# Kernel tuning notes

Measured on AMD Instinct MI355X. Metric: run time of the kernel, lower is better.

The kernel has to match this reference:

```python
import jax, jax.numpy as jnp
import numpy as np

GAMMA = 1.0
BIG = 1e10  # finite stand-in for +inf boundary; exp(-BIG) underflows to exactly 0 (grad-safe)


def setup_inputs() -> dict:
    key = jax.random.key(0)
    k1, k2 = jax.random.split(key)
    B, L, C = 64, 1024, 64
    x = jax.random.normal(k1, (B, L, C), dtype=jnp.float32)
    y = jax.random.normal(k2, (B, L, C), dtype=jnp.float32)
    return {"x": x, "y": y}


def _soft_dtw(x, y, gamma=GAMMA):
    B, L, C = x.shape
    # squared-euclidean pairwise cost, scaled by 1/gamma (matches torch code)
    x2 = jnp.sum(x * x, axis=-1)[:, :, None]            # [B,L,1]
    y2 = jnp.sum(y * y, axis=-1)[:, None, :]            # [B,1,L]
    D = (x2 + y2 - 2.0 * jnp.einsum('blc,bmc->blm', x, y)) / gamma  # [B,L,L]

    # Anti-diagonal wavefront DP over the (L+2)x(L+2) R matrix.
    # r_d[i] holds R[i, d-i] for the diagonal i+j=d, i in 0..L+1.
    n = L + 2
    ii = jnp.arange(n)
    i_idx = jnp.clip(ii - 1, 0, L - 1)
    r_prev2 = jnp.full((B, n), BIG, dtype=x.dtype).at[:, 0].set(0.0)  # diag d=0: R[0,0]=0
    r_prev1 = jnp.full((B, n), BIG, dtype=x.dtype)                    # diag d=1: all boundary
    big_col = jnp.full((B, 1), BIG, dtype=x.dtype)

    def step(carry, d):
        rp2, rp1 = carry
        jj = d - ii
        valid = (ii >= 1) & (ii <= L) & (jj >= 1) & (jj <= L)
        j_idx = jnp.clip(jj - 1, 0, L - 1)
        d_vals = D[:, i_idx, j_idx]                                   # [B,n] cost along diagonal
        r_diag = jnp.concatenate([big_col, rp2[:, :-1]], axis=1)      # R[i-1, j-1]
        r_up   = jnp.concatenate([big_col, rp1[:, :-1]], axis=1)      # R[i-1, j]
        r_left = rp1                                                  # R[i,   j-1]
        z = jnp.stack([-r_diag, -r_up, -r_left], axis=-1)             # [B,n,3]
        zmax = jnp.max(z, axis=-1)
        softmin = -(jnp.log(jnp.sum(jnp.exp(z - zmax[..., None]), axis=-1)) + zmax)
        new = jnp.where(valid[None, :], d_vals + softmin, BIG)
        return (rp1, new), None

    (_, r_last), _ = jax.lax.scan(step, (r_prev2, r_prev1), jnp.arange(2, 2 * L + 1))
    # last diagonal is d=2L; R[L,L] sits at index i=L
    return r_last[:, L] * gamma


def reference(x, y):
    return _soft_dtw(x, y)
```

## Files before the change

kernel.cpp:

```cpp
#include <hip/hip_runtime.h>


typedef unsigned short ushort_t;
typedef __attribute__((ext_vector_type(8))) short short8;
typedef __attribute__((ext_vector_type(4))) float f32x4;
typedef __attribute__((ext_vector_type(4))) unsigned short ushort4v;

constexpr int B_ = 64, L_ = 1024, C_ = 64;
constexpr int DSTR = 130;
constexpr int HBSTR = 1280;

#define BIGV 1e10f
#define INV_LN2 1.44269504088896340736f
#define LN2F 0.69314718055994530942f
#define DPP_WAVE_SHL1 0x130
#define DPP_WAVE_SHR1 0x138

static __device__ __forceinline__ ushort_t f2bf(float f) {
  unsigned u = __builtin_bit_cast(unsigned, f);
  unsigned r = (u + 0x7fffu + ((u >> 16) & 1u)) >> 16;
  return (ushort_t)r;
}
static __device__ __forceinline__ float exp2_(float x) {
  float r; asm("v_exp_f32 %0, %1" : "=v"(r) : "v"(x)); return r;
}
static __device__ __forceinline__ float log2_(float x) {
  float r; asm("v_log_f32 %0, %1" : "=v"(r) : "v"(x)); return r;
}
static __device__ __forceinline__ unsigned cvt_pk_bf16(float lo, float hi) {
  unsigned r; asm("v_cvt_pk_bf16_f32 %0, %1, %2" : "=v"(r) : "v"(lo), "v"(hi)); return r;
}
static __device__ __forceinline__ float dpp_shr1(float old, float src) {
  return __builtin_bit_cast(float, __builtin_amdgcn_update_dpp(
      __builtin_bit_cast(int, old), __builtin_bit_cast(int, src),
      DPP_WAVE_SHR1, 0xF, 0xF, false));
}
static __device__ __forceinline__ float dpp_shl1(float v) {
  return __builtin_bit_cast(float, __builtin_amdgcn_update_dpp(
      __builtin_bit_cast(int, v), __builtin_bit_cast(int, v),
      DPP_WAVE_SHL1, 0xF, 0xF, false));
}

__global__ __launch_bounds__(256) void prep_kernel(
    const float* __restrict__ x, const float* __restrict__ y,
    ushort_t* __restrict__ xb, ushort_t* __restrict__ yb,
    float* __restrict__ x2, float* __restrict__ y2, int* __restrict__ flagsG)
{
  if (blockIdx.x == 0 && threadIdx.x < 192) flagsG[threadIdx.x] = 0;
  const int lane = threadIdx.x & 63;
  const int sub = lane >> 4;
  const int cg  = lane & 15;
  const int wv = (blockIdx.x * blockDim.x + threadIdx.x) >> 6;
  const int nw = (gridDim.x * blockDim.x) >> 6;
  const int totalGroups = (2 * B_ * L_) >> 2;
  for (int g = wv; g < totalGroups; g += nw) {
    int r = g * 4 + sub;
    const float* src; ushort_t* dst; float* nrm;
    if (r < B_ * L_) { src = x; dst = xb; nrm = x2; }
    else             { r -= B_ * L_; src = y; dst = yb; nrm = y2; }
    const float4 v = *(const float4*)(src + (size_t)r * C_ + cg * 4);
    ushort4v p;
    p.x = f2bf(v.x); p.y = f2bf(v.y); p.z = f2bf(v.z); p.w = f2bf(v.w);
    *(ushort4v*)(dst + (size_t)r * C_ + cg * 4) = p;
    float s = v.x*v.x + v.y*v.y + v.z*v.z + v.w*v.w;
    s += __shfl_xor(s, 1); s += __shfl_xor(s, 2);
    s += __shfl_xor(s, 4); s += __shfl_xor(s, 8);
    if (cg == 0) nrm[r] = s * INV_LN2;
  }
}

template<int HDST, bool FIRST>
static __device__ __forceinline__ void dp_chunk(
    const int t, const int lane, float& cur, float& dgp, float hvv,
    const float zsel, const ushort_t* __restrict__ DtwLane,
    float* __restrict__ HbDst, float* __restrict__ HXB)
{
  const unsigned* pw = (const unsigned*)(DtwLane + ((t << 6) & 127));
  const int cb = (t << 6) - 63;
  unsigned a0 = pw[0], a1 = pw[1], b0 = pw[2], b1 = pw[3];

  auto step = [&](unsigned dw, int k, int u) -> float {
    float dv = __builtin_bit_cast(float, (k & 1) ? (dw & 0xffff0000u) : (dw << 16));
    float up = dpp_shr1(hvv, cur);
    float dg = dgp, lf = cur;
    if constexpr (FIRST) {
      bool at0 = (u == lane);
      dg = at0 ? zsel : dg;
      lf = at0 ? BIGV : lf;
    }
    float mn = fminf(fminf(up, dg), lf);
    float e = exp2_(mn - up) + exp2_(mn - dg) + exp2_(mn - lf);
    float nv = (dv + mn) - log2_(e);
    dgp = up;
    hvv = dpp_shl1(hvv);
    if constexpr (FIRST) { if (u >= lane) cur = nv; }
    else cur = nv;
    return nv;
  };
  auto flush4 = [&](int c0, float v0, float v1, float v2, float v3) {
    if constexpr (HDST == 0) {
      if (lane == 63) { HbDst[c0] = v0; HbDst[c0+1] = v1; HbDst[c0+2] = v2; HbDst[c0+3] = v3; }
    } else if constexpr (HDST == 1) {
      if (lane == 63) { HXB[c0] = v0; HXB[c0+1] = v1; HXB[c0+2] = v2; HXB[c0+3] = v3; }
    }
  };

  #pragma unroll 1
  for (int g = 0; g < 8; ++g) {
    const int u0 = g * 8;
    unsigned n0 = 0, n1 = 0, n2 = 0, n3 = 0;
    if (g < 7) {
      n0 = pw[u0/2 + 4]; n1 = pw[u0/2 + 5]; n2 = pw[u0/2 + 6]; n3 = pw[u0/2 + 7];
    }
    float v0 = step(a0, 0, u0 + 0);
    float v1 = step(a0, 1, u0 + 1);
    float v2 = step(a1, 0, u0 + 2);
    float v3 = step(a1, 1, u0 + 3);
    if constexpr (!FIRST) flush4(cb + u0, v0, v1, v2, v3);
    float v4 = step(b0, 0, u0 + 4);
    float v5 = step(b0, 1, u0 + 5);
    float v6 = step(b1, 0, u0 + 6);
    float v7 = step(b1, 1, u0 + 7);
    if constexpr (!FIRST) flush4(cb + u0 + 4, v4, v5, v6, v7);
    a0 = n0; a1 = n1; b0 = n2; b1 = n3;
    (void)v0; (void)v1; (void)v2; (void)v3; (void)v4; (void)v5; (void)v6; (void)v7;
  }
  if constexpr (FIRST) {
    if constexpr (HDST == 0) { if (lane == 63) HbDst[0] = cur; }
    else if constexpr (HDST == 1) { if (lane == 63) HXB[0] = cur; }
  }
}

template<int HDST>
static __device__ __forceinline__ void dp_tail(
    const int lane, float& cur, float& dgp,
    const ushort_t* __restrict__ DtwLane,
    float* __restrict__ HbDst, float* __restrict__ HXB)
{
  const unsigned* pw = (const unsigned*)(DtwLane);
  #pragma unroll 1
  for (int g = 0; g < 8; ++g) {
    unsigned w0 = pw[g*4], w1 = pw[g*4+1], w2 = pw[g*4+2], w3 = pw[g*4+3];
    #pragma unroll
    for (int k = 0; k < 8; ++k) {
      const int u = g * 8 + k;
      unsigned dw = (k < 2) ? w0 : (k < 4) ? w1 : (k < 6) ? w2 : w3;
      float dv = __builtin_bit_cast(float, (k & 1) ? (dw & 0xffff0000u) : (dw << 16));
      float up = dpp_shr1(BIGV, cur);
      float dg = dgp, lf = cur;
      float mn = fminf(fminf(up, dg), lf);
      float e = exp2_(mn - up) + exp2_(mn - dg) + exp2_(mn - lf);
      float nv = (dv + mn) - log2_(e);
      dgp = up;
      if (u < lane) {
        cur = nv;
        if constexpr (HDST == 0) { if (lane == 63) HbDst[961 + u] = nv; }
        else if constexpr (HDST == 1) { if (lane == 63) HXB[961 + u] = nv; }
      }
    }
  }
}

static __device__ __forceinline__ void spin_lds(int* f, int v) {
  int k = 0;
  while (__hip_atomic_load(f, __ATOMIC_ACQUIRE, __HIP_MEMORY_SCOPE_WORKGROUP) < v) {
    __builtin_amdgcn_s_sleep(1);
    if (++k > (1 << 26)) break;
  }
}
static __device__ __forceinline__ void spin_glb(int* f, int v) {
  int k = 0;
  while (__hip_atomic_load(f, __ATOMIC_ACQUIRE, __HIP_MEMORY_SCOPE_AGENT) < v) {
    __builtin_amdgcn_s_sleep(8);
    if (++k > (1 << 26)) break;
  }
}

template<int HSRC, int HDST>
static __device__ __forceinline__ void run_band(
    const ushort_t* __restrict__ xbB, const ushort_t* __restrict__ ybB,
    const float* __restrict__ x2B, const float* __restrict__ y2B,
    const float* __restrict__ HXin, float* __restrict__ HXout,
    int* __restrict__ fGin, int* __restrict__ fGout,
    ushort_t* __restrict__ Dtw, const float* __restrict__ HbSrc,
    float* __restrict__ HbDst, int* __restrict__ cin, int* __restrict__ cout,
    const int lane, const int W, float* __restrict__ outp)
{
  const int m = lane & 15, q = lane >> 4;
  const int i0 = W * 64;

  short8 af[4][2];
  #pragma unroll
  for (int mt = 0; mt < 4; ++mt)
    #pragma unroll
    for (int ks = 0; ks < 2; ++ks)
      af[mt][ks] = *(const short8*)(xbB + (size_t)(i0 + mt * 16 + m) * C_ + ks * 32 + q * 8);
  f32x4 x2q[4];
  #pragma unroll
  for (int mt = 0; mt < 4; ++mt) x2q[mt] = *(const f32x4*)(x2B + i0 + mt * 16 + q * 4);

  short8 bfr0[4], bfr1[4];
  auto load_bfr = [&](int tc) {
    const ushort_t* yb0 = ybB + (size_t)tc * 64 * C_;
    #pragma unroll
    for (int nt = 0; nt < 4; ++nt) {
      bfr0[nt] = *(const short8*)(yb0 + (size_t)(nt * 16 + m) * C_ + q * 8);
      bfr1[nt] = *(const short8*)(yb0 + (size_t)(nt * 16 + m) * C_ + 32 + q * 8);
    }
  };
  auto gram = [&](int tc) {
    const int cb = tc * 64;
    const float* y2j = y2B + cb;
    #pragma unroll
    for (int mt = 0; mt < 4; ++mt) {
      const int r0 = mt * 16 + q * 4;
      #pragma unroll
      for (int nt = 0; nt < 4; ++nt) {
        f32x4 acc = {0.f, 0.f, 0.f, 0.f};
        acc = __builtin_amdgcn_mfma_f32_16x16x32_bf16(af[mt][0], bfr0[nt], acc, 0, 0, 0);
        acc = __builtin_amdgcn_mfma_f32_16x16x32_bf16(af[mt][1], bfr1[nt], acc, 0, 0, 0);
        float y2v = y2j[nt * 16 + m];
        float d0 = fmaf(acc[0], -2.f * INV_LN2, x2q[mt][0] + y2v);
        float d1 = fmaf(acc[1], -2.f * INV_LN2, x2q[mt][1] + y2v);
        float d2 = fmaf(acc[2], -2.f * INV_LN2, x2q[mt][2] + y2v);
        float d3 = fmaf(acc[3], -2.f * INV_LN2, x2q[mt][3] + y2v);
        unsigned p01 = cvt_pk_bf16(d0, d1);
        unsigned p23 = cvt_pk_bf16(d2, d3);
        const int cs = cb + nt * 16 + m + r0;
        ushort_t* base = Dtw + r0 * DSTR;
        base[             ( cs      & 127)] = (ushort_t)p01;
        base[    DSTR  +  ((cs + 1) & 127)] = (ushort_t)(p01 >> 16);
        base[2 * DSTR  +  ((cs + 2) & 127)] = (ushort_t)p23;
        base[3 * DSTR  +  ((cs + 3) & 127)] = (ushort_t)(p23 >> 16);
      }
    }
  };

  float cur = 0.f, dgp = BIGV;
  const float zsel = (W == 0 && lane == 0) ? 0.f : BIGV;
  const ushort_t* DtwLane = Dtw + lane * DSTR;

  load_bfr(0);
  gram(0);

  #pragma unroll 1
  for (int t = 0; t < 16; ++t) {
    if (t < 15) load_bfr(t + 1);
    float hvv;
    if constexpr (HSRC == 0) {
      hvv = BIGV;
    } else if constexpr (HSRC == 1) {
      spin_lds(cin, t + 1);
      hvv = HbSrc[(t << 6) + lane];
    } else {
      spin_glb(fGin, t + 1);
      hvv = HXin[(t << 6) + lane];
    }
    if (t == 0) dp_chunk<HDST, true >(0, lane, cur, dgp, hvv, zsel, DtwLane, HbDst, HXout);
    else        dp_chunk<HDST, false>(t, lane, cur, dgp, hvv, zsel, DtwLane, HbDst, HXout);
    if constexpr (HDST == 0) {
      if (lane == 0) __hip_atomic_store(cout, t, __ATOMIC_RELEASE, __HIP_MEMORY_SCOPE_WORKGROUP);
    } else if constexpr (HDST == 1) {
      if (lane == 0) __hip_atomic_store(fGout, t, __ATOMIC_RELEASE, __HIP_MEMORY_SCOPE_AGENT);
    }
    if (t < 15) gram(t + 1);
  }
  dp_tail<HDST>(lane, cur, dgp, DtwLane, HbDst, HXout);
  if constexpr (HDST == 0) {
    if (lane == 0) __hip_atomic_store(cout, 16, __ATOMIC_RELEASE, __HIP_MEMORY_SCOPE_WORKGROUP);
  } else if constexpr (HDST == 1) {
    if (lane == 0) __hip_atomic_store(fGout, 16, __ATOMIC_RELEASE, __HIP_MEMORY_SCOPE_AGENT);
  }
  if (W == 15 && lane == 63) *outp = cur * LN2F;
}

__global__ __launch_bounds__(256) void sdtw_kernel(
    const ushort_t* __restrict__ xb, const ushort_t* __restrict__ yb,
    const float* __restrict__ x2g, const float* __restrict__ y2g,
    float* __restrict__ HXg, int* __restrict__ flagsG,
    float* __restrict__ out)
{
  __shared__ ushort_t Dt[4][64 * DSTR];
  __shared__ float Hb[3][HBSTR];
  __shared__ int cflag[4];

  const int b = blockIdx.x & 63;
  const int sub = blockIdx.x >> 6;
  const int w = threadIdx.x >> 6;
  const int lane = threadIdx.x & 63;
  const int W = sub * 4 + w;

  if (threadIdx.x < 4) cflag[threadIdx.x] = 0;
  __syncthreads();

  const ushort_t* xbB = xb + (size_t)b * L_ * C_;
  const ushort_t* ybB = yb + (size_t)b * L_ * C_;
  const float* x2B = x2g + b * L_;
  const float* y2B = y2g + b * L_;
  const float* HXin = HXg + ((size_t)b * 3 + (sub - 1)) * L_;
  float* HXout      = HXg + ((size_t)b * 3 + sub) * L_;
  int* fGin  = flagsG + b * 3 + (sub - 1);
  int* fGout = flagsG + b * 3 + sub;
  ushort_t* Dtw = &Dt[w][0];
  const float* HbSrc = (w > 0) ? &Hb[w - 1][0] : &Hb[0][0];
  float* HbDst = (w < 3) ? &Hb[w][0] : &Hb[0][0];
  int* cin  = (w > 0) ? &cflag[w - 1] : &cflag[0];
  int* cout = (w < 3) ? &cflag[w] : &cflag[3];
  float* outp = out + b;

  if (sub == 0) {
    if (w == 0)      run_band<0, 0>(xbB, ybB, x2B, y2B, HXin, HXout, fGin, fGout, Dtw, HbSrc, HbDst, cin, cout, lane, W, outp);
    else if (w < 3)  run_band<1, 0>(xbB, ybB, x2B, y2B, HXin, HXout, fGin, fGout, Dtw, HbSrc, HbDst, cin, cout, lane, W, outp);
    else             run_band<1, 1>(xbB, ybB, x2B, y2B, HXin, HXout, fGin, fGout, Dtw, HbSrc, HbDst, cin, cout, lane, W, outp);
  } else if (sub < 3) {
    if (w == 0)      run_band<2, 0>(xbB, ybB, x2B, y2B, HXin, HXout, fGin, fGout, Dtw, HbSrc, HbDst, cin, cout, lane, W, outp);
    else if (w < 3)  run_band<1, 0>(xbB, ybB, x2B, y2B, HXin, HXout, fGin, fGout, Dtw, HbSrc, HbDst, cin, cout, lane, W, outp);
    else             run_band<1, 1>(xbB, ybB, x2B, y2B, HXin, HXout, fGin, fGout, Dtw, HbSrc, HbDst, cin, cout, lane, W, outp);
  } else {
    if (w == 0)      run_band<2, 0>(xbB, ybB, x2B, y2B, HXin, HXout, fGin, fGout, Dtw, HbSrc, HbDst, cin, cout, lane, W, outp);
    else if (w < 3)  run_band<1, 0>(xbB, ybB, x2B, y2B, HXin, HXout, fGin, fGout, Dtw, HbSrc, HbDst, cin, cout, lane, W, outp);
    else             run_band<1, 2>(xbB, ybB, x2B, y2B, HXin, HXout, fGin, fGout, Dtw, HbSrc, HbDst, cin, cout, lane, W, outp);
  }
}

extern "C" void kernel_launch(void* const* d_in, const int* in_sizes, int n_in,
                              void* d_out, int out_size, void* d_ws, size_t ws_size,
                              hipStream_t stream) {
  const float* x = (const float*)d_in[0];
  const float* y = (const float*)d_in[1];
  float* out = (float*)d_out;

  char* ws = (char*)d_ws;
  const size_t XB = (size_t)B_ * L_ * C_ * 2;
  const size_t NB = (size_t)B_ * L_ * 4;
  ushort_t* xb = (ushort_t*)ws;
  ushort_t* yb = (ushort_t*)(ws + XB);
  float* x2 = (float*)(ws + 2 * XB);
  float* y2 = (float*)(ws + 2 * XB + NB);
  float* HX = (float*)(ws + 2 * XB + 2 * NB);
  int* flagsG = (int*)(ws + 2 * XB + 2 * NB + (size_t)B_ * 3 * L_ * 4);

  prep_kernel<<<512, 256, 0, stream>>>(x, y, xb, yb, x2, y2, flagsG);
  sdtw_kernel<<<256, 256, 0, stream>>>(xb, yb, x2, y2, HX, flagsG, out);
}
```

Measured before the change: 355.3 us.

## Interleave Gram MFMA into DP steps and use fine-grained intra-block handoff flags

```diff
diff --git a/kernel.cpp b/kernel.cpp
--- a/kernel.cpp
+++ b/kernel.cpp
@@ -13,32 +13,28 @@
 #define BIGV 1e10f
 #define INV_LN2 1.44269504088896340736f
 #define LN2F 0.69314718055994530942f
-#define DPP_WAVE_SHL1 0x130
-#define DPP_WAVE_SHR1 0x138
+
+template<int N> struct IC { static constexpr int v = N; };
+template<int I, int N, class F>
+static __device__ __forceinline__ void sfor(F&& f) {
+  if constexpr (I < N) { f(IC<I>{}); sfor<I + 1, N>(f); }
+}
 
 static __device__ __forceinline__ ushort_t f2bf(float f) {
   unsigned u = __builtin_bit_cast(unsigned, f);
   unsigned r = (u + 0x7fffu + ((u >> 16) & 1u)) >> 16;
   return (ushort_t)r;
 }
-static __device__ __forceinline__ float exp2_(float x) {
-  float r; asm("v_exp_f32 %0, %1" : "=v"(r) : "v"(x)); return r;
-}
-static __device__ __forceinline__ float log2_(float x) {
-  float r; asm("v_log_f32 %0, %1" : "=v"(r) : "v"(x)); return r;
-}
 static __device__ __forceinline__ unsigned cvt_pk_bf16(float lo, float hi) {
   unsigned r; asm("v_cvt_pk_bf16_f32 %0, %1, %2" : "=v"(r) : "v"(lo), "v"(hi)); return r;
 }
 static __device__ __forceinline__ float dpp_shr1(float old, float src) {
   return __builtin_bit_cast(float, __builtin_amdgcn_update_dpp(
-      __builtin_bit_cast(int, old), __builtin_bit_cast(int, src),
-      DPP_WAVE_SHR1, 0xF, 0xF, false));
+      __builtin_bit_cast(int, old), __builtin_bit_cast(int, src), 0x138, 0xF, 0xF, false));
 }
 static __device__ __forceinline__ float dpp_shl1(float v) {
   return __builtin_bit_cast(float, __builtin_amdgcn_update_dpp(
-      __builtin_bit_cast(int, v), __builtin_bit_cast(int, v),
-      DPP_WAVE_SHL1, 0xF, 0xF, false));
+      __builtin_bit_cast(int, v), __builtin_bit_cast(int, v), 0x130, 0xF, 0xF, false));
 }
 
 __global__ __launch_bounds__(256) void prep_kernel(
@@ -69,98 +65,6 @@
   }
 }
 
-template<int HDST, bool FIRST>
-static __device__ __forceinline__ void dp_chunk(
-    const int t, const int lane, float& cur, float& dgp, float hvv,
-    const float zsel, const ushort_t* __restrict__ DtwLane,
-    float* __restrict__ HbDst, float* __restrict__ HXB)
-{
-  const unsigned* pw = (const unsigned*)(DtwLane + ((t << 6) & 127));
-  const int cb = (t << 6) - 63;
-  unsigned a0 = pw[0], a1 = pw[1], b0 = pw[2], b1 = pw[3];
-
-  auto step = [&](unsigned dw, int k, int u) -> float {
-    float dv = __builtin_bit_cast(float, (k & 1) ? (dw & 0xffff0000u) : (dw << 16));
-    float up = dpp_shr1(hvv, cur);
-    float dg = dgp, lf = cur;
-    if constexpr (FIRST) {
-      bool at0 = (u == lane);
-      dg = at0 ? zsel : dg;
-      lf = at0 ? BIGV : lf;
-    }
-    float mn = fminf(fminf(up, dg), lf);
-    float e = exp2_(mn - up) + exp2_(mn - dg) + exp2_(mn - lf);
-    float nv = (dv + mn) - log2_(e);
-    dgp = up;
-    hvv = dpp_shl1(hvv);
-    if constexpr (FIRST) { if (u >= lane) cur = nv; }
-    else cur = nv;
-    return nv;
-  };
-  auto flush4 = [&](int c0, float v0, float v1, float v2, float v3) {
-    if constexpr (HDST == 0) {
-      if (lane == 63) { HbDst[c0] = v0; HbDst[c0+1] = v1; HbDst[c0+2] = v2; HbDst[c0+3] = v3; }
-    } else if constexpr (HDST == 1) {
-      if (lane == 63) { HXB[c0] = v0; HXB[c0+1] = v1; HXB[c0+2] = v2; HXB[c0+3] = v3; }
-    }
-  };
-
-  #pragma unroll 1
-  for (int g = 0; g < 8; ++g) {
-    const int u0 = g * 8;
-    unsigned n0 = 0, n1 = 0, n2 = 0, n3 = 0;
-    if (g < 7) {
-      n0 = pw[u0/2 + 4]; n1 = pw[u0/2 + 5]; n2 = pw[u0/2 + 6]; n3 = pw[u0/2 + 7];
-    }
-    float v0 = step(a0, 0, u0 + 0);
-    float v1 = step(a0, 1, u0 + 1);
-    float v2 = step(a1, 0, u0 + 2);
-    float v3 = step(a1, 1, u0 + 3);
-    if constexpr (!FIRST) flush4(cb + u0, v0, v1, v2, v3);
-    float v4 = step(b0, 0, u0 + 4);
-    float v5 = step(b0, 1, u0 + 5);
-    float v6 = step(b1, 0, u0 + 6);
-    float v7 = step(b1, 1, u0 + 7);
-    if constexpr (!FIRST) flush4(cb + u0 + 4, v4, v5, v6, v7);
-    a0 = n0; a1 = n1; b0 = n2; b1 = n3;
-    (void)v0; (void)v1; (void)v2; (void)v3; (void)v4; (void)v5; (void)v6; (void)v7;
-  }
-  if constexpr (FIRST) {
-    if constexpr (HDST == 0) { if (lane == 63) HbDst[0] = cur; }
-    else if constexpr (HDST == 1) { if (lane == 63) HXB[0] = cur; }
-  }
-}
-
-template<int HDST>
-static __device__ __forceinline__ void dp_tail(
-    const int lane, float& cur, float& dgp,
-    const ushort_t* __restrict__ DtwLane,
-    float* __restrict__ HbDst, float* __restrict__ HXB)
-{
-  const unsigned* pw = (const unsigned*)(DtwLane);
-  #pragma unroll 1
-  for (int g = 0; g < 8; ++g) {
-    unsigned w0 = pw[g*4], w1 = pw[g*4+1], w2 = pw[g*4+2], w3 = pw[g*4+3];
-    #pragma unroll
-    for (int k = 0; k < 8; ++k) {
-      const int u = g * 8 + k;
-      unsigned dw = (k < 2) ? w0 : (k < 4) ? w1 : (k < 6) ? w2 : w3;
-      float dv = __builtin_bit_cast(float, (k & 1) ? (dw & 0xffff0000u) : (dw << 16));
-      float up = dpp_shr1(BIGV, cur);
-      float dg = dgp, lf = cur;
-      float mn = fminf(fminf(up, dg), lf);
-      float e = exp2_(mn - up) + exp2_(mn - dg) + exp2_(mn - lf);
-      float nv = (dv + mn) - log2_(e);
-      dgp = up;
-      if (u < lane) {
-        cur = nv;
-        if constexpr (HDST == 0) { if (lane == 63) HbDst[961 + u] = nv; }
-        else if constexpr (HDST == 1) { if (lane == 63) HXB[961 + u] = nv; }
-      }
-    }
-  }
-}
-
 static __device__ __forceinline__ void spin_lds(int* f, int v) {
   int k = 0;
   while (__hip_atomic_load(f, __ATOMIC_ACQUIRE, __HIP_MEMORY_SCOPE_WORKGROUP) < v) {
@@ -171,7 +75,7 @@
 static __device__ __forceinline__ void spin_glb(int* f, int v) {
   int k = 0;
   while (__hip_atomic_load(f, __ATOMIC_ACQUIRE, __HIP_MEMORY_SCOPE_AGENT) < v) {
-    __builtin_amdgcn_s_sleep(8);
+    __builtin_amdgcn_s_sleep(2);
     if (++k > (1 << 26)) break;
   }
 }
@@ -183,10 +87,11 @@
     const float* __restrict__ HXin, float* __restrict__ HXout,
     int* __restrict__ fGin, int* __restrict__ fGout,
     ushort_t* __restrict__ Dtw, const float* __restrict__ HbSrc,
-    float* __restrict__ HbDst, int* __restrict__ cin, int* __restrict__ cout,
+    float* __restrict__ HbDst, float* __restrict__ HScr,
+    int* __restrict__ cin, int* __restrict__ cout,
     const int lane, const int W, float* __restrict__ outp)
 {
-  const int m = lane & 15, q = lane >> 4;
+  const int m = lane & 15, q = lane >> 4, l7 = lane & 7;
   const int i0 = W * 64;
 
   short8 af[4][2];
@@ -200,77 +105,189 @@
   for (int mt = 0; mt < 4; ++mt) x2q[mt] = *(const f32x4*)(x2B + i0 + mt * 16 + q * 4);
 
   short8 bfr0[4], bfr1[4];
+  f32x4 y2r = {0.f, 0.f, 0.f, 0.f};
   auto load_bfr = [&](int tc) {
     const ushort_t* yb0 = ybB + (size_t)tc * 64 * C_;
     #pragma unroll
     for (int nt = 0; nt < 4; ++nt) {
       bfr0[nt] = *(const short8*)(yb0 + (size_t)(nt * 16 + m) * C_ + q * 8);
       bfr1[nt] = *(const short8*)(yb0 + (size_t)(nt * 16 + m) * C_ + 32 + q * 8);
-    }
-  };
-  auto gram = [&](int tc) {
-    const int cb = tc * 64;
-    const float* y2j = y2B + cb;
-    #pragma unroll
-    for (int mt = 0; mt < 4; ++mt) {
-      const int r0 = mt * 16 + q * 4;
+      y2r[nt] = y2B[tc * 64 + nt * 16 + m];
+    }
+  };
+
+  auto gram_pair = [&](auto PC, const int gcb) {
+    constexpr int p = decltype(PC)::v;
+    constexpr int mt = p >> 2;
+    constexpr int nt = p & 3;
+    f32x4 acc = {0.f, 0.f, 0.f, 0.f};
+    acc = __builtin_amdgcn_mfma_f32_16x16x32_bf16(af[mt][0], bfr0[nt], acc, 0, 0, 0);
+    acc = __builtin_amdgcn_mfma_f32_16x16x32_bf16(af[mt][1], bfr1[nt], acc, 0, 0, 0);
+    const float y2v = y2r[nt];
+    float d0 = fmaf(acc[0], -2.f * INV_LN2, x2q[mt][0] + y2v);
+    float d1 = fmaf(acc[1], -2.f * INV_LN2, x2q[mt][1] + y2v);
+    float d2 = fmaf(acc[2], -2.f * INV_LN2, x2q[mt][2] + y2v);
+    float d3 = fmaf(acc[3], -2.f * INV_LN2, x2q[mt][3] + y2v);
+    unsigned p01 = cvt_pk_bf16(d0, d1);
+    unsigned p23 = cvt_pk_bf16(d2, d3);
+    const int rr = mt * 16 + q * 4;
+    const int cs = gcb + nt * 16 + m + rr;
+    ushort_t* base = Dtw + rr * DSTR;
+    base[            ( cs      & 127)] = (ushort_t)p01;
+    base[    DSTR +  ((cs + 1) & 127)] = (ushort_t)(p01 >> 16);
+    base[2 * DSTR +  ((cs + 2) & 127)] = (ushort_t)p23;
+    base[3 * DSTR +  ((cs + 3) & 127)] = (ushort_t)(p23 >> 16);
+  };
+
+  float cur = 0.f, dgp = BIGV, hvv = BIGV;
+  const float zsel = (W == 0 && lane == 0) ? 0.0f : BIGV;
+  const ushort_t* DtLane = Dtw + lane * DSTR;
+
+  auto dp_chunk = [&](auto FC, auto GC, const int t) {
+    constexpr bool FIRST  = decltype(FC)::v != 0;
+    constexpr bool DOGRAM = decltype(GC)::v != 0;
+    const unsigned* pw = (const unsigned*)(DtLane + ((t << 6) & 127));
+    const int cb = (t << 6) - 63;
+    const int gcb = (t + 1) << 6;
+
+    if constexpr (HSRC == 2) {
+      spin_glb(fGin, t + 1);
+      HScr[lane] = HXin[(t << 6) + lane];
+    }
+
+    unsigned d0 = pw[0], d1 = pw[1], d2 = pw[2], d3 = pw[3];
+
+    auto step = [&](unsigned dw, int k, int u) -> float {
+      float dv = __builtin_bit_cast(float, (k & 1) ? (dw & 0xffff0000u) : (dw << 16));
+      float up = dpp_shr1(hvv, cur);
+      float dg = dgp, lf = cur;
+      if constexpr (FIRST) {
+        bool at0 = (u == lane);
+        dg = at0 ? zsel : dg;
+        lf = at0 ? BIGV : lf;
+      }
+      float mn = fminf(fminf(up, dg), lf);
+      float e = __builtin_amdgcn_exp2f(mn - up) + __builtin_amdgcn_exp2f(mn - dg)
+              + __builtin_amdgcn_exp2f(mn - lf);
+      float nv = (dv + mn) - __builtin_amdgcn_logf(e);
+      dgp = up;
+      if constexpr (HSRC != 0) hvv = dpp_shl1(hvv);
+      if constexpr (FIRST) { if (u >= lane) cur = nv; }
+      else cur = nv;
+      return nv;
+    };
+    auto flush4 = [&](int c0, float v0, float v1, float v2, float v3) {
+      if constexpr (HDST == 0) {
+        if (lane == 63) { HbDst[c0] = v0; HbDst[c0+1] = v1; HbDst[c0+2] = v2; HbDst[c0+3] = v3; }
+      } else if constexpr (HDST == 1) {
+        if (lane == 63) { HXout[c0] = v0; HXout[c0+1] = v1; HXout[c0+2] = v2; HXout[c0+3] = v3; }
+      }
+    };
+
+    sfor<0, 8>([&](auto GG) {
+      constexpr int g = decltype(GG)::v;
+      if constexpr (HSRC == 1) {
+        if constexpr ((g & 1) == 0) spin_lds(cin, (t << 6) + (g << 3) + 16);
+        hvv = HbSrc[(t << 6) + (g << 3) + l7];
+      } else if constexpr (HSRC == 2) {
+        hvv = HScr[(g << 3) + l7];
+      }
+      unsigned n0 = 0, n1 = 0, n2 = 0, n3 = 0;
+      if constexpr (g < 7) {
+        n0 = pw[4*g+4]; n1 = pw[4*g+5]; n2 = pw[4*g+6]; n3 = pw[4*g+7];
+      }
+      const int u0 = g << 3;
+      float v0 = step(d0, 0, u0 + 0);
+      float v1 = step(d0, 1, u0 + 1);
+      float v2 = step(d1, 0, u0 + 2);
+      float v3 = step(d1, 1, u0 + 3);
+      if constexpr (!FIRST) flush4(cb + u0, v0, v1, v2, v3);
+      float v4 = step(d2, 0, u0 + 4);
+      float v5 = step(d2, 1, u0 + 5);
+      float v6 = step(d3, 0, u0 + 6);
+      float v7 = step(d3, 1, u0 + 7);
+      if constexpr (!FIRST) flush4(cb + u0 + 4, v4, v5, v6, v7);
+      if constexpr (DOGRAM) {
+        gram_pair(IC<2*g>{}, gcb);
+        gram_pair(IC<2*g+1>{}, gcb);
+      }
+      if constexpr (HDST == 0 && !FIRST) {
+        if constexpr ((g & 1) == 1) {
+          if (lane == 0)
+            __hip_atomic_store(cout, (t << 6) + (g << 3) - 55,
+                               __ATOMIC_RELEASE, __HIP_MEMORY_SCOPE_WORKGROUP);
+        }
+      }
+      d0 = n0; d1 = n1; d2 = n2; d3 = n3;
+      (void)v0;(void)v1;(void)v2;(void)v3;(void)v4;(void)v5;(void)v6;(void)v7;
+    });
+    if constexpr (FIRST) {
+      if (lane == 63) {
+        if constexpr (HDST == 0) HbDst[0] = cur;
+        else if constexpr (HDST == 1) HXout[0] = cur;
+      }
+      if constexpr (HDST == 0) {
+        if (lane == 0)
+          __hip_atomic_store(cout, 1, __ATOMIC_RELEASE, __HIP_MEMORY_SCOPE_WORKGROUP);
+      }
+    }
+  };
+
+  auto signal_glb = [&](int v) {
+    if constexpr (HDST == 1) {
+      if (lane == 0) __hip_atomic_store(fGout, v, __ATOMIC_RELEASE, __HIP_MEMORY_SCOPE_AGENT);
+    }
+  };
+
+  auto dp_tail = [&]() {
+    const unsigned* pw = (const unsigned*)DtLane;
+    #pragma unroll 1
+    for (int g = 0; g < 8; ++g) {
+      unsigned w0 = pw[g*4], w1 = pw[g*4+1], w2 = pw[g*4+2], w3 = pw[g*4+3];
       #pragma unroll
-      for (int nt = 0; nt < 4; ++nt) {
-        f32x4 acc = {0.f, 0.f, 0.f, 0.f};
-        acc = __builtin_amdgcn_mfma_f32_16x16x32_bf16(af[mt][0], bfr0[nt], acc, 0, 0, 0);
-        acc = __builtin_amdgcn_mfma_f32_16x16x32_bf16(af[mt][1], bfr1[nt], acc, 0, 0, 0);
-        float y2v = y2j[nt * 16 + m];
-        float d0 = fmaf(acc[0], -2.f * INV_LN2, x2q[mt][0] + y2v);
-        float d1 = fmaf(acc[1], -2.f * INV_LN2, x2q[mt][1] + y2v);
-        float d2 = fmaf(acc[2], -2.f * INV_LN2, x2q[mt][2] + y2v);
-        float d3 = fmaf(acc[3], -2.f * INV_LN2, x2q[mt][3] + y2v);
-        unsigned p01 = cvt_pk_bf16(d0, d1);
-        unsigned p23 = cvt_pk_bf16(d2, d3);
-        const int cs = cb + nt * 16 + m + r0;
-        ushort_t* base = Dtw + r0 * DSTR;
-        base[             ( cs      & 127)] = (ushort_t)p01;
-        base[    DSTR  +  ((cs + 1) & 127)] = (ushort_t)(p01 >> 16);
-        base[2 * DSTR  +  ((cs + 2) & 127)] = (ushort_t)p23;
-        base[3 * DSTR  +  ((cs + 3) & 127)] = (ushort_t)(p23 >> 16);
-      }
-    }
-  };
-
-  float cur = 0.f, dgp = BIGV;
-  const float zsel = (W == 0 && lane == 0) ? 0.f : BIGV;
-  const ushort_t* DtwLane = Dtw + lane * DSTR;
+      for (int k = 0; k < 8; ++k) {
+        const int u = g * 8 + k;
+        unsigned dw = (k < 2) ? w0 : (k < 4) ? w1 : (k < 6) ? w2 : w3;
+        float dv = __builtin_bit_cast(float, (k & 1) ? (dw & 0xffff0000u) : (dw << 16));
+        float up = dpp_shr1(BIGV, cur);
+        float dg = dgp, lf = cur;
+        float mn = fminf(fminf(up, dg), lf);
+        float e = __builtin_amdgcn_exp2f(mn - up) + __builtin_amdgcn_exp2f(mn - dg)
+                + __builtin_amdgcn_exp2f(mn - lf);
+        float nv = (dv + mn) - __builtin_amdgcn_logf(e);
+        dgp = up;
+        if (u < lane) {
+          cur = nv;
+          if (lane == 63) {
+            if constexpr (HDST == 0) HbDst[961 + u] = nv;
+            else if constexpr (HDST == 1) HXout[961 + u] = nv;
+          }
+        }
+      }
+      if constexpr (HDST == 0) {
+        if (lane == 0)
+          __hip_atomic_store(cout, (g < 7) ? (969 + 8 * g) : 1024,
+                             __ATOMIC_RELEASE, __HIP_MEMORY_SCOPE_WORKGROUP);
+      }
+    }
+  };
 
   load_bfr(0);
-  gram(0);
-
+  sfor<0, 16>([&](auto PC) { gram_pair(PC, 0); });
+
+  load_bfr(1);
+  dp_chunk(IC<1>{}, IC<1>{}, 0);
+  signal_glb(0);
   #pragma unroll 1
-  for (int t = 0; t < 16; ++t) {
-    if (t < 15) load_bfr(t + 1);
-    float hvv;
-    if constexpr (HSRC == 0) {
-      hvv = BIGV;
-    } else if constexpr (HSRC == 1) {
-      spin_lds(cin, t + 1);
-      hvv = HbSrc[(t << 6) + lane];
-    } else {
-      spin_glb(fGin, t + 1);
-      hvv = HXin[(t << 6) + lane];
-    }
-    if (t == 0) dp_chunk<HDST, true >(0, lane, cur, dgp, hvv, zsel, DtwLane, HbDst, HXout);
-    else        dp_chunk<HDST, false>(t, lane, cur, dgp, hvv, zsel, DtwLane, HbDst, HXout);
-    if constexpr (HDST == 0) {
-      if (lane == 0) __hip_atomic_store(cout, t, __ATOMIC_RELEASE, __HIP_MEMORY_SCOPE_WORKGROUP);
-    } else if constexpr (HDST == 1) {
-      if (lane == 0) __hip_atomic_store(fGout, t, __ATOMIC_RELEASE, __HIP_MEMORY_SCOPE_AGENT);
-    }
-    if (t < 15) gram(t + 1);
-  }
-  dp_tail<HDST>(lane, cur, dgp, DtwLane, HbDst, HXout);
-  if constexpr (HDST == 0) {
-    if (lane == 0) __hip_atomic_store(cout, 16, __ATOMIC_RELEASE, __HIP_MEMORY_SCOPE_WORKGROUP);
-  } else if constexpr (HDST == 1) {
-    if (lane == 0) __hip_atomic_store(fGout, 16, __ATOMIC_RELEASE, __HIP_MEMORY_SCOPE_AGENT);
-  }
+  for (int t = 1; t <= 14; ++t) {
+    load_bfr(t + 1);
+    dp_chunk(IC<0>{}, IC<1>{}, t);
+    signal_glb(t);
+  }
+  dp_chunk(IC<0>{}, IC<0>{}, 15);
+  signal_glb(15);
+  dp_tail();
+  signal_glb(16);
   if (W == 15 && lane == 63) *outp = cur * LN2F;
 }
 
@@ -282,6 +299,7 @@
 {
   __shared__ ushort_t Dt[4][64 * DSTR];
   __shared__ float Hb[3][HBSTR];
+  __shared__ float HScr[64];
   __shared__ int cflag[4];
 
   const int b = blockIdx.x & 63;
@@ -297,10 +315,10 @@
   const ushort_t* ybB = yb + (size_t)b * L_ * C_;
   const float* x2B = x2g + b * L_;
   const float* y2B = y2g + b * L_;
-  const float* HXin = HXg + ((size_t)b * 3 + (sub - 1)) * L_;
-  float* HXout      = HXg + ((size_t)b * 3 + sub) * L_;
-  int* fGin  = flagsG + b * 3 + (sub - 1);
-  int* fGout = flagsG + b * 3 + sub;
+  const float* HXin = HXg + ((size_t)b * 3 + (sub > 0 ? sub - 1 : 0)) * L_;
+  float* HXout      = HXg + ((size_t)b * 3 + (sub < 3 ? sub : 2)) * L_;
+  int* fGin  = flagsG + b * 3 + (sub > 0 ? sub - 1 : 0);
+  int* fGout = flagsG + b * 3 + (sub < 3 ? sub : 2);
   ushort_t* Dtw = &Dt[w][0];
   const float* HbSrc = (w > 0) ? &Hb[w - 1][0] : &Hb[0][0];
   float* HbDst = (w < 3) ? &Hb[w][0] : &Hb[0][0];
@@ -309,17 +327,17 @@
   float* outp = out + b;
 
   if (sub == 0) {
-    if (w == 0)      run_band<0, 0>(xbB, ybB, x2B, y2B, HXin, HXout, fGin, fGout, Dtw, HbSrc, HbDst, cin, cout, lane, W, outp);
-    else if (w < 3)  run_band<1, 0>(xbB, ybB, x2B, y2B, HXin, HXout, fGin, fGout, Dtw, HbSrc, HbDst, cin, cout, lane, W, outp);
-    else             run_band<1, 1>(xbB, ybB, x2B, y2B, HXin, HXout, fGin, fGout, Dtw, HbSrc, HbDst, cin, cout, lane, W, outp);
+    if (w == 0)      run_band<0, 0>(xbB, ybB, x2B, y2B, HXin, HXout, fGin, fGout, Dtw, HbSrc, HbDst, HScr, cin, cout, lane, W, outp);
+    else if (w < 3)  run_band<1, 0>(xbB, ybB, x2B, y2B, HXin, HXout, fGin, fGout, Dtw, HbSrc, HbDst, HScr, cin, cout, lane, W, outp);
+    else             run_band<1, 1>(xbB, ybB, x2B, y2B, HXin, HXout, fGin, fGout, Dtw, HbSrc, HbDst, HScr, cin, cout, lane, W, outp);
   } else if (sub < 3) {
-    if (w == 0)      run_band<2, 0>(xbB, ybB, x2B, y2B, HXin, HXout, fGin, fGout, Dtw, HbSrc, HbDst, cin, cout, lane, W, outp);
-    else if (w < 3)  run_band<1, 0>(xbB, ybB, x2B, y2B, HXin, HXout, fGin, fGout, Dtw, HbSrc, HbDst, cin, cout, lane, W, outp);
-    else             run_band<1, 1>(xbB, ybB, x2B, y2B, HXin, HXout, fGin, fGout, Dtw, HbSrc, HbDst, cin, cout, lane, W, outp);
+    if (w == 0)      run_band<2, 0>(xbB, ybB, x2B, y2B, HXin, HXout, fGin, fGout, Dtw, HbSrc, HbDst, HScr, cin, cout, lane, W, outp);
+    else if (w < 3)  run_band<1, 0>(xbB, ybB, x2B, y2B, HXin, HXout, fGin, fGout, Dtw, HbSrc, HbDst, HScr, cin, cout, lane, W, outp);
+    else             run_band<1, 1>(xbB, ybB, x2B, y2B, HXin, HXout, fGin, fGout, Dtw, HbSrc, HbDst, HScr, cin, cout, lane, W, outp);
   } else {
-    if (w == 0)      run_band<2, 0>(xbB, ybB, x2B, y2B, HXin, HXout, fGin, fGout, Dtw, HbSrc, HbDst, cin, cout, lane, W, outp);
-    else if (w < 3)  run_band<1, 0>(xbB, ybB, x2B, y2B, HXin, HXout, fGin, fGout, Dtw, HbSrc, HbDst, cin, cout, lane, W, outp);
-    else             run_band<1, 2>(xbB, ybB, x2B, y2B, HXin, HXout, fGin, fGout, Dtw, HbSrc, HbDst, cin, cout, lane, W, outp);
+    if (w == 0)      run_band<2, 0>(xbB, ybB, x2B, y2B, HXin, HXout, fGin, fGout, Dtw, HbSrc, HbDst, HScr, cin, cout, lane, W, outp);
+    else if (w < 3)  run_band<1, 0>(xbB, ybB, x2B, y2B, HXin, HXout, fGin, fGout, Dtw, HbSrc, HbDst, HScr, cin, cout, lane, W, outp);
+    else             run_band<1, 2>(xbB, ybB, x2B, y2B, HXin, HXout, fGin, fGout, Dtw, HbSrc, HbDst, HScr, cin, cout, lane, W, outp);
   }
 }
 
```

Result: slower. 431.8 us (+21.5%).

## Signal wavefront handoff between waves every 8 columns instead of per chunk

Applied to the files above, without the earlier changes.

```diff
diff --git a/kernel.cpp b/kernel.cpp
--- a/kernel.cpp
+++ b/kernel.cpp
@@ -13,32 +13,24 @@
 #define BIGV 1e10f
 #define INV_LN2 1.44269504088896340736f
 #define LN2F 0.69314718055994530942f
-#define DPP_WAVE_SHL1 0x130
-#define DPP_WAVE_SHR1 0x138
+
+template<int N> struct IC { static constexpr int v = N; };
 
 static __device__ __forceinline__ ushort_t f2bf(float f) {
   unsigned u = __builtin_bit_cast(unsigned, f);
   unsigned r = (u + 0x7fffu + ((u >> 16) & 1u)) >> 16;
   return (ushort_t)r;
 }
-static __device__ __forceinline__ float exp2_(float x) {
-  float r; asm("v_exp_f32 %0, %1" : "=v"(r) : "v"(x)); return r;
-}
-static __device__ __forceinline__ float log2_(float x) {
-  float r; asm("v_log_f32 %0, %1" : "=v"(r) : "v"(x)); return r;
-}
 static __device__ __forceinline__ unsigned cvt_pk_bf16(float lo, float hi) {
   unsigned r; asm("v_cvt_pk_bf16_f32 %0, %1, %2" : "=v"(r) : "v"(lo), "v"(hi)); return r;
 }
 static __device__ __forceinline__ float dpp_shr1(float old, float src) {
   return __builtin_bit_cast(float, __builtin_amdgcn_update_dpp(
-      __builtin_bit_cast(int, old), __builtin_bit_cast(int, src),
-      DPP_WAVE_SHR1, 0xF, 0xF, false));
+      __builtin_bit_cast(int, old), __builtin_bit_cast(int, src), 0x138, 0xF, 0xF, false));
 }
 static __device__ __forceinline__ float dpp_shl1(float v) {
   return __builtin_bit_cast(float, __builtin_amdgcn_update_dpp(
-      __builtin_bit_cast(int, v), __builtin_bit_cast(int, v),
-      DPP_WAVE_SHL1, 0xF, 0xF, false));
+      __builtin_bit_cast(int, v), __builtin_bit_cast(int, v), 0x130, 0xF, 0xF, false));
 }
 
 __global__ __launch_bounds__(256) void prep_kernel(
@@ -69,98 +61,6 @@
   }
 }
 
-template<int HDST, bool FIRST>
-static __device__ __forceinline__ void dp_chunk(
-    const int t, const int lane, float& cur, float& dgp, float hvv,
-    const float zsel, const ushort_t* __restrict__ DtwLane,
-    float* __restrict__ HbDst, float* __restrict__ HXB)
-{
-  const unsigned* pw = (const unsigned*)(DtwLane + ((t << 6) & 127));
-  const int cb = (t << 6) - 63;
-  unsigned a0 = pw[0], a1 = pw[1], b0 = pw[2], b1 = pw[3];
-
-  auto step = [&](unsigned dw, int k, int u) -> float {
-    float dv = __builtin_bit_cast(float, (k & 1) ? (dw & 0xffff0000u) : (dw << 16));
-    float up = dpp_shr1(hvv, cur);
-    float dg = dgp, lf = cur;
-    if constexpr (FIRST) {
-      bool at0 = (u == lane);
-      dg = at0 ? zsel : dg;
-      lf = at0 ? BIGV : lf;
-    }
-    float mn = fminf(fminf(up, dg), lf);
-    float e = exp2_(mn - up) + exp2_(mn - dg) + exp2_(mn - lf);
-    float nv = (dv + mn) - log2_(e);
-    dgp = up;
-    hvv = dpp_shl1(hvv);
-    if constexpr (FIRST) { if (u >= lane) cur = nv; }
-    else cur = nv;
-    return nv;
-  };
-  auto flush4 = [&](int c0, float v0, float v1, float v2, float v3) {
-    if constexpr (HDST == 0) {
-      if (lane == 63) { HbDst[c0] = v0; HbDst[c0+1] = v1; HbDst[c0+2] = v2; HbDst[c0+3] = v3; }
-    } else if constexpr (HDST == 1) {
-      if (lane == 63) { HXB[c0] = v0; HXB[c0+1] = v1; HXB[c0+2] = v2; HXB[c0+3] = v3; }
-    }
-  };
-
-  #pragma unroll 1
-  for (int g = 0; g < 8; ++g) {
-    const int u0 = g * 8;
-    unsigned n0 = 0, n1 = 0, n2 = 0, n3 = 0;
-    if (g < 7) {
-      n0 = pw[u0/2 + 4]; n1 = pw[u0/2 + 5]; n2 = pw[u0/2 + 6]; n3 = pw[u0/2 + 7];
-    }
-    float v0 = step(a0, 0, u0 + 0);
-    float v1 = step(a0, 1, u0 + 1);
-    float v2 = step(a1, 0, u0 + 2);
-    float v3 = step(a1, 1, u0 + 3);
-    if constexpr (!FIRST) flush4(cb + u0, v0, v1, v2, v3);
-    float v4 = step(b0, 0, u0 + 4);
-    float v5 = step(b0, 1, u0 + 5);
-    float v6 = step(b1, 0, u0 + 6);
-    float v7 = step(b1, 1, u0 + 7);
-    if constexpr (!FIRST) flush4(cb + u0 + 4, v4, v5, v6, v7);
-    a0 = n0; a1 = n1; b0 = n2; b1 = n3;
-    (void)v0; (void)v1; (void)v2; (void)v3; (void)v4; (void)v5; (void)v6; (void)v7;
-  }
-  if constexpr (FIRST) {
-    if constexpr (HDST == 0) { if (lane == 63) HbDst[0] = cur; }
-    else if constexpr (HDST == 1) { if (lane == 63) HXB[0] = cur; }
-  }
-}
-
-template<int HDST>
-static __device__ __forceinline__ void dp_tail(
-    const int lane, float& cur, float& dgp,
-    const ushort_t* __restrict__ DtwLane,
-    float* __restrict__ HbDst, float* __restrict__ HXB)
-{
-  const unsigned* pw = (const unsigned*)(DtwLane);
-  #pragma unroll 1
-  for (int g = 0; g < 8; ++g) {
-    unsigned w0 = pw[g*4], w1 = pw[g*4+1], w2 = pw[g*4+2], w3 = pw[g*4+3];
-    #pragma unroll
-    for (int k = 0; k < 8; ++k) {
-      const int u = g * 8 + k;
-      unsigned dw = (k < 2) ? w0 : (k < 4) ? w1 : (k < 6) ? w2 : w3;
-      float dv = __builtin_bit_cast(float, (k & 1) ? (dw & 0xffff0000u) : (dw << 16));
-      float up = dpp_shr1(BIGV, cur);
-      float dg = dgp, lf = cur;
-      float mn = fminf(fminf(up, dg), lf);
-      float e = exp2_(mn - up) + exp2_(mn - dg) + exp2_(mn - lf);
-      float nv = (dv + mn) - log2_(e);
-      dgp = up;
-      if (u < lane) {
-        cur = nv;
-        if constexpr (HDST == 0) { if (lane == 63) HbDst[961 + u] = nv; }
-        else if constexpr (HDST == 1) { if (lane == 63) HXB[961 + u] = nv; }
-      }
-    }
-  }
-}
-
 static __device__ __forceinline__ void spin_lds(int* f, int v) {
   int k = 0;
   while (__hip_atomic_load(f, __ATOMIC_ACQUIRE, __HIP_MEMORY_SCOPE_WORKGROUP) < v) {
@@ -171,7 +71,7 @@
 static __device__ __forceinline__ void spin_glb(int* f, int v) {
   int k = 0;
   while (__hip_atomic_load(f, __ATOMIC_ACQUIRE, __HIP_MEMORY_SCOPE_AGENT) < v) {
-    __builtin_amdgcn_s_sleep(8);
+    __builtin_amdgcn_s_sleep(2);
     if (++k > (1 << 26)) break;
   }
 }
@@ -186,7 +86,7 @@
     float* __restrict__ HbDst, int* __restrict__ cin, int* __restrict__ cout,
     const int lane, const int W, float* __restrict__ outp)
 {
-  const int m = lane & 15, q = lane >> 4;
+  const int m = lane & 15, q = lane >> 4, l7 = lane & 7;
   const int i0 = W * 64;
 
   short8 af[4][2];
@@ -237,40 +137,156 @@
   };
 
   float cur = 0.f, dgp = BIGV;
-  const float zsel = (W == 0 && lane == 0) ? 0.f : BIGV;
-  const ushort_t* DtwLane = Dtw + lane * DSTR;
+  float hvvC = BIGV, hvvN = BIGV;
+  int fseen = 0;
+  const float zsel = (W == 0 && lane == 0) ? 0.0f : BIGV;
+  const ushort_t* DtLane = Dtw + lane * DSTR;
 
   load_bfr(0);
   gram(0);
 
+  if constexpr (HSRC == 1) {
+    spin_lds(cin, 16);
+    hvvC = HbSrc[l7];
+    fseen = __hip_atomic_load(cin, __ATOMIC_RELAXED, __HIP_MEMORY_SCOPE_WORKGROUP);
+  }
+
+  auto dp_chunk = [&](auto FC, const int t) {
+    constexpr bool FIRST = decltype(FC)::v != 0;
+    const unsigned* pw = (const unsigned*)(DtLane + ((t << 6) & 127));
+    const int cb = (t << 6) - 63;
+
+    if constexpr (HSRC == 2) {
+      spin_glb(fGin, t + 1);
+      hvvC = HXin[(t << 6) + lane];
+    }
+    unsigned a0 = pw[0], a1 = pw[1], b0 = pw[2], b1 = pw[3];
+
+    auto step = [&](unsigned dw, int k, int u) -> float {
+      float dv = __builtin_bit_cast(float, (k & 1) ? (dw & 0xffff0000u) : (dw << 16));
+      float up = dpp_shr1(hvvC, cur);
+      float dg = dgp, lf = cur;
+      if constexpr (FIRST) {
+        bool at0 = (u == lane);
+        dg = at0 ? zsel : dg;
+        lf = at0 ? BIGV : lf;
+      }
+      float mn = fminf(fminf(up, dg), lf);
+      float e = __builtin_amdgcn_exp2f(mn - up) + __builtin_amdgcn_exp2f(mn - dg)
+              + __builtin_amdgcn_exp2f(mn - lf);
+      float nv = (dv + mn) - __builtin_amdgcn_logf(e);
+      dgp = up;
+      if constexpr (HSRC != 0) hvvC = dpp_shl1(hvvC);
+      if constexpr (FIRST) { if (u >= lane) cur = nv; }
+      else cur = nv;
+      return nv;
+    };
+    auto flush4 = [&](int c0, float v0, float v1, float v2, float v3) {
+      if constexpr (HDST == 0) {
+        if (lane == 63) { HbDst[c0] = v0; HbDst[c0+1] = v1; HbDst[c0+2] = v2; HbDst[c0+3] = v3; }
+      } else if constexpr (HDST == 1) {
+        if (lane == 63) { HXout[c0] = v0; HXout[c0+1] = v1; HXout[c0+2] = v2; HXout[c0+3] = v3; }
+      }
+    };
+
+    #pragma unroll 1
+    for (int g = 0; g < 8; ++g) {
+      const int u0 = g * 8;
+      const int s0 = (t << 6) + u0;
+      if constexpr (HSRC == 1) {
+        const int need = (s0 + 16 < 1024) ? (s0 + 16) : 1024;
+        if (fseen < need) { spin_lds(cin, need); fseen = need; }
+        asm volatile("" ::: "memory");
+        int ha = s0 + 8 + l7; if (ha > 1023) ha = 1023;
+        hvvN = HbSrc[ha];
+        fseen = __hip_atomic_load(cin, __ATOMIC_RELAXED, __HIP_MEMORY_SCOPE_WORKGROUP);
+      }
+      unsigned n0 = 0, n1 = 0, n2 = 0, n3 = 0;
+      if (g < 7) {
+        n0 = pw[u0/2 + 4]; n1 = pw[u0/2 + 5]; n2 = pw[u0/2 + 6]; n3 = pw[u0/2 + 7];
+      }
+      float v0 = step(a0, 0, u0 + 0);
+      float v1 = step(a0, 1, u0 + 1);
+      float v2 = step(a1, 0, u0 + 2);
+      float v3 = step(a1, 1, u0 + 3);
+      if constexpr (!FIRST) flush4(cb + u0, v0, v1, v2, v3);
+      float v4 = step(b0, 0, u0 + 4);
+      float v5 = step(b0, 1, u0 + 5);
+      float v6 = step(b1, 0, u0 + 6);
+      float v7 = step(b1, 1, u0 + 7);
+      if constexpr (!FIRST) flush4(cb + u0 + 4, v4, v5, v6, v7);
+      if constexpr (HDST == 0 && !FIRST) {
+        if (lane == 0)
+          __hip_atomic_store(cout, s0 - 55, __ATOMIC_RELEASE, __HIP_MEMORY_SCOPE_WORKGROUP);
+      }
+      if constexpr (HSRC == 1) hvvC = hvvN;
+      a0 = n0; a1 = n1; b0 = n2; b1 = n3;
+      (void)v0; (void)v1; (void)v2; (void)v3; (void)v4; (void)v5; (void)v6; (void)v7;
+    }
+    if constexpr (FIRST) {
+      if (lane == 63) {
+        if constexpr (HDST == 0) HbDst[0] = cur;
+        else if constexpr (HDST == 1) HXout[0] = cur;
+      }
+      if constexpr (HDST == 0) {
+        if (lane == 0)
+          __hip_atomic_store(cout, 1, __ATOMIC_RELEASE, __HIP_MEMORY_SCOPE_WORKGROUP);
+      }
+    }
+  };
+
+  auto signal_glb = [&](int v) {
+    if constexpr (HDST == 1) {
+      if (lane == 0) __hip_atomic_store(fGout, v, __ATOMIC_RELEASE, __HIP_MEMORY_SCOPE_AGENT);
+    }
+  };
+
+  auto dp_tail = [&]() {
+    const unsigned* pw = (const unsigned*)DtLane;
+    #pragma unroll 1
+    for (int g = 0; g < 8; ++g) {
+      unsigned w0 = pw[g*4], w1 = pw[g*4+1], w2 = pw[g*4+2], w3 = pw[g*4+3];
+      #pragma unroll
+      for (int k = 0; k < 8; ++k) {
+        const int u = g * 8 + k;
+        unsigned dw = (k < 2) ? w0 : (k < 4) ? w1 : (k < 6) ? w2 : w3;
+        float dv = __builtin_bit_cast(float, (k & 1) ? (dw & 0xffff0000u) : (dw << 16));
+        float up = dpp_shr1(BIGV, cur);
+        float dg = dgp, lf = cur;
+        float mn = fminf(fminf(up, dg), lf);
+        float e = __builtin_amdgcn_exp2f(mn - up) + __builtin_amdgcn_exp2f(mn - dg)
+                + __builtin_amdgcn_exp2f(mn - lf);
+        float nv = (dv + mn) - __builtin_amdgcn_logf(e);
+        dgp = up;
+        if (u < lane) {
+          cur = nv;
+          if (lane == 63) {
+            if constexpr (HDST == 0) HbDst[961 + u] = nv;
+            else if constexpr (HDST == 1) HXout[961 + u] = nv;
+          }
+        }
+      }
+      if constexpr (HDST == 0) {
+        if (lane == 0)
+          __hip_atomic_store(cout, (g < 7) ? (969 + 8 * g) : 1024,
+                             __ATOMIC_RELEASE, __HIP_MEMORY_SCOPE_WORKGROUP);
+      }
+    }
+  };
+
+  load_bfr(1);
+  dp_chunk(IC<1>{}, 0);
+  signal_glb(0);
+  gram(1);
   #pragma unroll 1
-  for (int t = 0; t < 16; ++t) {
+  for (int t = 1; t < 16; ++t) {
     if (t < 15) load_bfr(t + 1);
-    float hvv;
-    if constexpr (HSRC == 0) {
-      hvv = BIGV;
-    } else if constexpr (HSRC == 1) {
-      spin_lds(cin, t + 1);
-      hvv = HbSrc[(t << 6) + lane];
-    } else {
-      spin_glb(fGin, t + 1);
-      hvv = HXin[(t << 6) + lane];
-    }
-    if (t == 0) dp_chunk<HDST, true >(0, lane, cur, dgp, hvv, zsel, DtwLane, HbDst, HXout);
-    else        dp_chunk<HDST, false>(t, lane, cur, dgp, hvv, zsel, DtwLane, HbDst, HXout);
-    if constexpr (HDST == 0) {
-      if (lane == 0) __hip_atomic_store(cout, t, __ATOMIC_RELEASE, __HIP_MEMORY_SCOPE_WORKGROUP);
-    } else if constexpr (HDST == 1) {
-      if (lane == 0) __hip_atomic_store(fGout, t, __ATOMIC_RELEASE, __HIP_MEMORY_SCOPE_AGENT);
-    }
+    dp_chunk(IC<0>{}, t);
+    signal_glb(t);
     if (t < 15) gram(t + 1);
   }
-  dp_tail<HDST>(lane, cur, dgp, DtwLane, HbDst, HXout);
-  if constexpr (HDST == 0) {
-    if (lane == 0) __hip_atomic_store(cout, 16, __ATOMIC_RELEASE, __HIP_MEMORY_SCOPE_WORKGROUP);
-  } else if constexpr (HDST == 1) {
-    if (lane == 0) __hip_atomic_store(fGout, 16, __ATOMIC_RELEASE, __HIP_MEMORY_SCOPE_AGENT);
-  }
+  dp_tail();
+  signal_glb(16);
   if (W == 15 && lane == 63) *outp = cur * LN2F;
 }
 
@@ -297,10 +313,10 @@
   const ushort_t* ybB = yb + (size_t)b * L_ * C_;
   const float* x2B = x2g + b * L_;
   const float* y2B = y2g + b * L_;
-  const float* HXin = HXg + ((size_t)b * 3 + (sub - 1)) * L_;
-  float* HXout      = HXg + ((size_t)b * 3 + sub) * L_;
-  int* fGin  = flagsG + b * 3 + (sub - 1);
-  int* fGout = flagsG + b * 3 + sub;
+  const float* HXin = HXg + ((size_t)b * 3 + (sub > 0 ? sub - 1 : 0)) * L_;
+  float* HXout      = HXg + ((size_t)b * 3 + (sub < 3 ? sub : 2)) * L_;
+  int* fGin  = flagsG + b * 3 + (sub > 0 ? sub - 1 : 0);
+  int* fGout = flagsG + b * 3 + (sub < 3 ? sub : 2);
   ushort_t* Dtw = &Dt[w][0];
   const float* HbSrc = (w > 0) ? &Hb[w - 1][0] : &Hb[0][0];
   float* HbDst = (w < 3) ? &Hb[w][0] : &Hb[0][0];
```

New measurement: 370.4 us. 4.2% more time.
